# Kernel tuning notes

Measured on AMD Instinct MI355X. Metric: run time of the kernel, lower is better.

Reference implementation:

```python
import jax, jax.numpy as jnp
import numpy as np

N = 100000
E = 1600000
F_IN = 128
HID = 64


def setup_inputs() -> dict:
    key = jax.random.key(0)
    ks = jax.random.split(key, 8)
    x = jax.random.normal(ks[0], (N, F_IN), dtype=jnp.float32)
    edge_index = jax.random.randint(ks[1], (2, E), 0, N, dtype=jnp.int32)
    # GCNConv params: weight [in, out] (glorot-ish scale), bias [out]
    W1 = jax.random.normal(ks[2], (F_IN, HID), dtype=jnp.float32) / np.sqrt(F_IN)
    b1 = jnp.zeros((HID,), dtype=jnp.float32)
    W2 = jax.random.normal(ks[3], (HID, HID), dtype=jnp.float32) / np.sqrt(HID)
    b2 = jnp.zeros((HID,), dtype=jnp.float32)
    Wc = jax.random.normal(ks[4], (HID, 1), dtype=jnp.float32) / np.sqrt(HID)
    bc = jnp.zeros((1,), dtype=jnp.float32)
    return {"x": x, "edge_index": edge_index, "W1": W1, "b1": b1,
            "W2": W2, "b2": b2, "Wc": Wc, "bc": bc}


def _gcn_conv(x, src, dst, W, b):
    # PyG GCNConv: h = x @ W, then symmetric-normalized aggregation over
    # edges with self-loops: out[d] = sum_e deg^-1/2[s] deg^-1/2[d] h[s] + b
    n = x.shape[0]
    h = x @ W                                            # [N, out]
    deg = jax.ops.segment_sum(jnp.ones_like(dst, dtype=h.dtype), dst,
                              num_segments=n)            # in-degree incl. self-loops
    dinv = jnp.where(deg > 0, jax.lax.rsqrt(deg), 0.0)   # [N]
    norm = dinv[src] * dinv[dst]                         # [E+N]
    msg = h[src] * norm[:, None]                         # gather + scale
    out = jax.ops.segment_sum(msg, dst, num_segments=n)  # scatter-add
    return out + b


def reference(x, edge_index, W1, b1, W2, b2, Wc, bc):
    n = x.shape[0]
    loop = jnp.arange(n, dtype=edge_index.dtype)
    src = jnp.concatenate([edge_index[0], loop])  # add self-loops
    dst = jnp.concatenate([edge_index[1], loop])
    h = jax.nn.relu(_gcn_conv(x, src, dst, W1, b1))  # dropout in eval mode = identity
    h = jax.nn.relu(_gcn_conv(h, src, dst, W2, b2))
    return (h @ Wc + bc).squeeze(-1)  # [N]
```

## Files before the change

kernel.cpp:

```cpp
#include <hip/hip_runtime.h>


#define FIN 128
#define HIDDEN 64
#define NBUCK 196
#define CAP 9216
#define EPB 8192

typedef __attribute__((ext_vector_type(8))) short bf16x8;
typedef __attribute__((ext_vector_type(4))) float f32x4;

__device__ __forceinline__ unsigned f2bf_pair(float a, float b) {
    unsigned ua = __float_as_uint(a);
    unsigned ub = __float_as_uint(b);
    ua = (ua + 0x7FFFu + ((ua >> 16) & 1u)) >> 16;
    ub = (ub + 0x7FFFu + ((ub >> 16) & 1u)) & 0xFFFF0000u;
    return ua | ub;
}
__device__ __forceinline__ unsigned short f2bf1(float a) {
    unsigned u = __float_as_uint(a);
    return (unsigned short)((u + 0x7FFFu + ((u >> 16) & 1u)) >> 16);
}
#define BF_LO(u) __uint_as_float((u) << 16)
#define BF_HI(u) __uint_as_float((u) & 0xFFFF0000u)

__global__ __launch_bounds__(256) void k_scatter_direct(const int* __restrict__ src,
                                                        const int* __restrict__ dst,
                                                        int* __restrict__ bcursor,
                                                        int* __restrict__ pairs, int e) {
    __shared__ int h[NBUCK], base_s[NBUCK], cur[NBUCK];
    int dloc[EPB / 256];
    int tid = threadIdx.x;
    if (tid < NBUCK) { h[tid] = 0; cur[tid] = 0; }
    __syncthreads();
    int start = blockIdx.x * EPB;
#pragma unroll
    for (int i = 0; i < EPB / 256; i++) {
        int idx = start + tid + i * 256;
        int d = (idx < e) ? dst[idx] : -1;
        dloc[i] = d;
        if (d >= 0) atomicAdd(&h[d >> 9], 1);
    }
    __syncthreads();
    if (tid < NBUCK && h[tid] > 0) base_s[tid] = atomicAdd(&bcursor[tid], h[tid]);
    __syncthreads();
#pragma unroll
    for (int i = 0; i < EPB / 256; i++) {
        int idx = start + tid + i * 256;
        int d = dloc[i];
        if (d >= 0) {
            int b = d >> 9;
            int pos = base_s[b] + atomicAdd(&cur[b], 1);
            if (pos < CAP) pairs[b * CAP + pos] = (src[idx] << 9) | (d & 511);
        }
    }
}

__global__ __launch_bounds__(256) void k_csr_bucket(const int* __restrict__ pairs,
                                                    const int* __restrict__ bcursor,
                                                    int2* __restrict__ rowinfo,
                                                    float* __restrict__ dinv,
                                                    int* __restrict__ csr_src, int n) {
    __shared__ int cnt[512];
    __shared__ int off[512];
    __shared__ int ws2[256];
    int tid = threadIdx.x;
    int b = blockIdx.x;
    int node0 = b << 9;
    cnt[tid] = 0; cnt[tid + 256] = 0;
    __syncthreads();
    int s0 = b * CAP;
    int s1 = s0 + min(bcursor[b], CAP);
    for (int i = s0 + tid; i < s1; i += 256) atomicAdd(&cnt[pairs[i] & 511], 1);
    __syncthreads();
    int c0 = cnt[2 * tid], c1 = cnt[2 * tid + 1];
    int tsum = c0 + c1;
    ws2[tid] = tsum;
    __syncthreads();
    for (int o = 1; o < 256; o <<= 1) {
        int x = 0;
        if (tid >= o) x = ws2[tid - o];
        __syncthreads();
        if (tid >= o) ws2[tid] += x;
        __syncthreads();
    }
    int excl = ws2[tid] - tsum;
    off[2 * tid] = excl;
    off[2 * tid + 1] = excl + c0;
    int n0 = node0 + 2 * tid, n1 = node0 + 2 * tid + 1;
    if (n0 < n) { rowinfo[n0] = make_int2(s0 + excl, c0);      dinv[n0] = rsqrtf((float)c0 + 1.0f); }
    if (n1 < n) { rowinfo[n1] = make_int2(s0 + excl + c0, c1); dinv[n1] = rsqrtf((float)c1 + 1.0f); }
    cnt[2 * tid] = 0; cnt[2 * tid + 1] = 0;
    __syncthreads();
    for (int i = s0 + tid; i < s1; i += 256) {
        int p = pairs[i];
        int l = p & 511;
        int pos = s0 + off[l] + atomicAdd(&cnt[l], 1);
        csr_src[pos] = p >> 9;
    }
}


__global__ __launch_bounds__(256) void k_mfma1(const float4* __restrict__ x4,
                                               const float* __restrict__ w1,
                                               const float* __restrict__ dinv,
                                               uint2* __restrict__ hsb, int n) {
    __shared__ unsigned short sW[64 * 136];
    int tid = threadIdx.x;
#pragma unroll
    for (int i = 0; i < 32; i++) {
        int idx = tid + i * 256;
        int k = idx >> 6, ch = idx & 63;
        sW[ch * 136 + k] = f2bf1(w1[idx]);
    }
    __syncthreads();
    int lane = tid & 63, wave = tid >> 6;
    int quad = lane >> 4, nl = lane & 15;
    int node = blockIdx.x * 64 + wave * 16 + nl;
    int ic = min(node, n - 1);
    const float4* px = x4 + (size_t)ic * 32 + quad * 2;
    bf16x8 bfr[4];
#pragma unroll
    for (int kc = 0; kc < 4; kc++) {
        float4 p = px[kc * 8];
        float4 q = px[kc * 8 + 1];
        union { unsigned u[4]; bf16x8 v; } t;
        t.u[0] = f2bf_pair(p.x, p.y); t.u[1] = f2bf_pair(p.z, p.w);
        t.u[2] = f2bf_pair(q.x, q.y); t.u[3] = f2bf_pair(q.z, q.w);
        bfr[kc] = t.v;
    }
    const bf16x8* sW8 = (const bf16x8*)sW;
    f32x4 a0 = {0.f, 0.f, 0.f, 0.f}, a1 = a0, a2 = a0, a3 = a0;
#pragma unroll
    for (int kc = 0; kc < 4; kc++) {
        int ko = kc * 4 + quad;
        bf16x8 w0 = sW8[(nl +  0) * 17 + ko];
        bf16x8 w1f = sW8[(nl + 16) * 17 + ko];
        bf16x8 w2f = sW8[(nl + 32) * 17 + ko];
        bf16x8 w3f = sW8[(nl + 48) * 17 + ko];
        a0 = __builtin_amdgcn_mfma_f32_16x16x32_bf16(w0,  bfr[kc], a0, 0, 0, 0);
        a1 = __builtin_amdgcn_mfma_f32_16x16x32_bf16(w1f, bfr[kc], a1, 0, 0, 0);
        a2 = __builtin_amdgcn_mfma_f32_16x16x32_bf16(w2f, bfr[kc], a2, 0, 0, 0);
        a3 = __builtin_amdgcn_mfma_f32_16x16x32_bf16(w3f, bfr[kc], a3, 0, 0, 0);
    }
    if (node < n) {
        float s = dinv[node];
        uint2* o = hsb + (size_t)node * 16 + quad;
        o[0]  = make_uint2(f2bf_pair(a0.x * s, a0.y * s), f2bf_pair(a0.z * s, a0.w * s));
        o[4]  = make_uint2(f2bf_pair(a1.x * s, a1.y * s), f2bf_pair(a1.z * s, a1.w * s));
        o[8]  = make_uint2(f2bf_pair(a2.x * s, a2.y * s), f2bf_pair(a2.z * s, a2.w * s));
        o[12] = make_uint2(f2bf_pair(a3.x * s, a3.y * s), f2bf_pair(a3.z * s, a3.w * s));
    }
}

__global__ __launch_bounds__(256) void k_agg1_gemm2(const int2* __restrict__ rowinfo,
                                                    const int* __restrict__ csr_src,
                                                    const uint4* __restrict__ hsb4,
                                                    const float* __restrict__ dinv,
                                                    const float4* __restrict__ b1_4,
                                                    const float* __restrict__ w2,
                                                    uint2* __restrict__ hsb2, int n) {
    __shared__ unsigned short sW[64 * 72];
    __shared__ float sV[16 * 68];
    int tid = threadIdx.x;
#pragma unroll
    for (int i = 0; i < 16; i++) {
        int idx = tid + i * 256;
        int k = idx >> 6, ch = idx & 63;
        sW[ch * 72 + k] = f2bf1(w2[idx]);
    }
    int lane = tid & 63;
    int node0 = blockIdx.x * 16;
    int nloc = tid >> 4;
    int node = node0 + nloc;
    int el = (lane >> 3) & 1, cq = lane & 7;
    if (node < n) {
        int2 rpd = rowinfo[node];
        int start = rpd.x, deg = rpd.y;
        int end = start + deg;
        float4 accA = make_float4(0.f, 0.f, 0.f, 0.f), accB = accA;
        int nr = (deg + 3) >> 2;
#pragma unroll 2
        for (int r = 0; r < nr; r++) {
            int base = start + (r << 2);
            int e0 = base + el;
            int e1 = base + 2 + el;
            int s0 = csr_src[min(e0, end - 1)];
            int s1 = csr_src[min(e1, end - 1)];
            float m0 = (e0 < end) ? 1.f : 0.f;
            float m1 = (e1 < end) ? 1.f : 0.f;
            uint4 g0 = hsb4[(size_t)s0 * 8 + cq];
            uint4 g1 = hsb4[(size_t)s1 * 8 + cq];
            accA.x += m0 * BF_LO(g0.x) + m1 * BF_LO(g1.x);
            accA.y += m0 * BF_HI(g0.x) + m1 * BF_HI(g1.x);
            accA.z += m0 * BF_LO(g0.y) + m1 * BF_LO(g1.y);
            accA.w += m0 * BF_HI(g0.y) + m1 * BF_HI(g1.y);
            accB.x += m0 * BF_LO(g0.z) + m1 * BF_LO(g1.z);
            accB.y += m0 * BF_HI(g0.z) + m1 * BF_HI(g1.z);
            accB.z += m0 * BF_LO(g0.w) + m1 * BF_LO(g1.w);
            accB.w += m0 * BF_HI(g0.w) + m1 * BF_HI(g1.w);
        }
        accA.x += __shfl_xor(accA.x, 8); accA.y += __shfl_xor(accA.y, 8);
        accA.z += __shfl_xor(accA.z, 8); accA.w += __shfl_xor(accA.w, 8);
        accB.x += __shfl_xor(accB.x, 8); accB.y += __shfl_xor(accB.y, 8);
        accB.z += __shfl_xor(accB.z, 8); accB.w += __shfl_xor(accB.w, 8);
        if (el == 0) {
            uint4 g = hsb4[(size_t)node * 8 + cq];
            float s = dinv[node];
            float4 bA = b1_4[cq * 2], bB = b1_4[cq * 2 + 1];
            float4 vA, vB;
            vA.x = fmaxf(s * (accA.x + BF_LO(g.x)) + bA.x, 0.f);
            vA.y = fmaxf(s * (accA.y + BF_HI(g.x)) + bA.y, 0.f);
            vA.z = fmaxf(s * (accA.z + BF_LO(g.y)) + bA.z, 0.f);
            vA.w = fmaxf(s * (accA.w + BF_HI(g.y)) + bA.w, 0.f);
            vB.x = fmaxf(s * (accB.x + BF_LO(g.z)) + bB.x, 0.f);
            vB.y = fmaxf(s * (accB.y + BF_HI(g.z)) + bB.y, 0.f);
            vB.z = fmaxf(s * (accB.z + BF_LO(g.w)) + bB.z, 0.f);
            vB.w = fmaxf(s * (accB.w + BF_HI(g.w)) + bB.w, 0.f);
            float* vb = sV + nloc * 68 + cq * 8;
            *(float4*)vb = vA;
            *(float4*)(vb + 4) = vB;
        }
    }
    __syncthreads();
    int wave = tid >> 6;
    int quad = lane >> 4, nl = lane & 15;
    const bf16x8* sW8 = (const bf16x8*)sW;
    f32x4 acc = {0.f, 0.f, 0.f, 0.f};
#pragma unroll
    for (int kc = 0; kc < 2; kc++) {
        const float* vb = sV + nl * 68 + kc * 32 + quad * 8;
        float4 p = *(const float4*)vb;
        float4 q = *(const float4*)(vb + 4);
        union { unsigned u[4]; bf16x8 v; } t;
        t.u[0] = f2bf_pair(p.x, p.y); t.u[1] = f2bf_pair(p.z, p.w);
        t.u[2] = f2bf_pair(q.x, q.y); t.u[3] = f2bf_pair(q.z, q.w);
        bf16x8 a = sW8[(wave * 16 + nl) * 9 + kc * 4 + quad];
        acc = __builtin_amdgcn_mfma_f32_16x16x32_bf16(a, t.v, acc, 0, 0, 0);
    }
    int onode = node0 + nl;
    if (onode < n) {
        float s = dinv[onode];
        hsb2[(size_t)onode * 16 + wave * 4 + quad] =
            make_uint2(f2bf_pair(acc.x * s, acc.y * s), f2bf_pair(acc.z * s, acc.w * s));
    }
}

__global__ __launch_bounds__(256) void k_agg2_head(const int2* __restrict__ rowinfo,
                                                   const int* __restrict__ csr_src,
                                                   const uint4* __restrict__ hsb4,
                                                   const float* __restrict__ dinv,
                                                   const float4* __restrict__ b2_4,
                                                   const float4* __restrict__ wc_4,
                                                   const float* __restrict__ bc,
                                                   float* __restrict__ out, int n) {
    int lane = threadIdx.x & 63;
    int node = (blockIdx.x * 256 + threadIdx.x) >> 4;
    if (node >= n) return;
    int el = (lane >> 3) & 1, cq = lane & 7;
    int2 rpd = rowinfo[node];
    int start = rpd.x, deg = rpd.y;
    int end = start + deg;
    float4 accA = make_float4(0.f, 0.f, 0.f, 0.f), accB = accA;
    int nr = (deg + 3) >> 2;
#pragma unroll 2
    for (int r = 0; r < nr; r++) {
        int base = start + (r << 2);
        int e0 = base + el;
        int e1 = base + 2 + el;
        int s0 = csr_src[min(e0, end - 1)];
        int s1 = csr_src[min(e1, end - 1)];
        float m0 = (e0 < end) ? 1.f : 0.f;
        float m1 = (e1 < end) ? 1.f : 0.f;
        uint4 g0 = hsb4[(size_t)s0 * 8 + cq];
        uint4 g1 = hsb4[(size_t)s1 * 8 + cq];
        accA.x += m0 * BF_LO(g0.x) + m1 * BF_LO(g1.x);
        accA.y += m0 * BF_HI(g0.x) + m1 * BF_HI(g1.x);
        accA.z += m0 * BF_LO(g0.y) + m1 * BF_LO(g1.y);
        accA.w += m0 * BF_HI(g0.y) + m1 * BF_HI(g1.y);
        accB.x += m0 * BF_LO(g0.z) + m1 * BF_LO(g1.z);
        accB.y += m0 * BF_HI(g0.z) + m1 * BF_HI(g1.z);
        accB.z += m0 * BF_LO(g0.w) + m1 * BF_LO(g1.w);
        accB.w += m0 * BF_HI(g0.w) + m1 * BF_HI(g1.w);
    }
    accA.x += __shfl_xor(accA.x, 8); accA.y += __shfl_xor(accA.y, 8);
    accA.z += __shfl_xor(accA.z, 8); accA.w += __shfl_xor(accA.w, 8);
    accB.x += __shfl_xor(accB.x, 8); accB.y += __shfl_xor(accB.y, 8);
    accB.z += __shfl_xor(accB.z, 8); accB.w += __shfl_xor(accB.w, 8);
    uint4 g = hsb4[(size_t)node * 8 + cq];
    float s = dinv[node];
    float4 bA = b2_4[cq * 2], bB = b2_4[cq * 2 + 1];
    float4 wA = wc_4[cq * 2], wB = wc_4[cq * 2 + 1];
    float t = fmaxf(s * (accA.x + BF_LO(g.x)) + bA.x, 0.f) * wA.x
            + fmaxf(s * (accA.y + BF_HI(g.x)) + bA.y, 0.f) * wA.y
            + fmaxf(s * (accA.z + BF_LO(g.y)) + bA.z, 0.f) * wA.z
            + fmaxf(s * (accA.w + BF_HI(g.y)) + bA.w, 0.f) * wA.w
            + fmaxf(s * (accB.x + BF_LO(g.z)) + bB.x, 0.f) * wB.x
            + fmaxf(s * (accB.y + BF_HI(g.z)) + bB.y, 0.f) * wB.y
            + fmaxf(s * (accB.z + BF_LO(g.w)) + bB.z, 0.f) * wB.z
            + fmaxf(s * (accB.w + BF_HI(g.w)) + bB.w, 0.f) * wB.w;
    t += __shfl_xor(t, 1);
    t += __shfl_xor(t, 2);
    t += __shfl_xor(t, 4);
    if ((lane & 15) == 0) out[node] = t + bc[0];
}

extern "C" void kernel_launch(void* const* d_in, const int* in_sizes, int n_in,
                              void* d_out, int out_size, void* d_ws, size_t ws_size,
                              hipStream_t stream) {
    const float* x  = (const float*)d_in[0];
    const int*   ei = (const int*)d_in[1];
    const float* W1 = (const float*)d_in[2];
    const float* b1 = (const float*)d_in[3];
    const float* W2 = (const float*)d_in[4];
    const float* b2 = (const float*)d_in[5];
    const float* Wc = (const float*)d_in[6];
    const float* bc = (const float*)d_in[7];
    int n = in_sizes[0] / FIN;
    int e = in_sizes[1] / 2;
    const int* srcv = ei;
    const int* dstv = ei + e;

    char* ws = (char*)d_ws;
    float* dinv    = (float*)(ws + 0);
    int2*  rowinfo = (int2*)(ws + (512u << 10));
    int*   csr_src = (int*)(ws + 1536u * 1024);
    int*   bcursor = (int*)(ws + 8800u * 1024);
    uint2* hsb1    = (uint2*)(ws + (9u << 20));
    uint2* hsb2    = (uint2*)(ws + (22u << 20));
    int*   pairs   = (int*)hsb2;

    int nb_sc   = (e + EPB - 1) / EPB;
    int nb_rows = (n + 63) / 64;
    int nb_agg  = (n + 15) / 16;

    hipMemsetAsync(bcursor, 0, NBUCK * sizeof(int), stream);
    k_scatter_direct<<<nb_sc, 256, 0, stream>>>(srcv, dstv, bcursor, pairs, e);
    k_csr_bucket<<<NBUCK, 256, 0, stream>>>(pairs, bcursor, rowinfo, dinv, csr_src, n);

    k_mfma1<<<nb_rows, 256, 0, stream>>>((const float4*)x, W1, dinv, hsb1, n);
    k_agg1_gemm2<<<nb_agg, 256, 0, stream>>>(rowinfo, csr_src, (const uint4*)hsb1,
                                             dinv, (const float4*)b1, W2, hsb2, n);
    k_agg2_head<<<nb_agg, 256, 0, stream>>>(rowinfo, csr_src, (const uint4*)hsb2,
                                            dinv, (const float4*)b2, (const float4*)Wc,
                                            bc, (float*)d_out, n);
}
```

Baseline: 215.9 us.

## Fuse edge scatter with first GEMM, move dinv scaling into aggregation

The edge bucketing scatter and the first x@W1 MFMA GEMM now run in one launch, with block ranges split by role. This is possible because the GEMM no longer pre-scales rows by dinv; instead the layer-1 aggregation gathers dinv[src] per edge and applies s^2 to the self term. Buckets shrink to 256 nodes (more buckets, smaller capacity), and both aggregation loops are unrolled to four neighbours per lane-pair per iteration. The goal is to overlap the GEMM with the scatter, remove a launch, and raise memory-level parallelism in the gathers, at the cost of an extra dinv gather per edge in layer 1.

Measured after the change: 211.0 us. 2.3% less time.

```diff
diff --git a/kernel.cpp b/kernel.cpp
--- a/kernel.cpp
+++ b/kernel.cpp
@@ -3,9 +3,9 @@
 
 #define FIN 128
 #define HIDDEN 64
-#define NBUCK 196
-#define CAP 9216
-#define EPB 8192
+#define NBUCK 391
+#define CAP 4608
+#define EPB 4096
 
 typedef __attribute__((ext_vector_type(8))) short bf16x8;
 typedef __attribute__((ext_vector_type(4))) float f32x4;
@@ -24,89 +24,48 @@
 #define BF_LO(u) __uint_as_float((u) << 16)
 #define BF_HI(u) __uint_as_float((u) & 0xFFFF0000u)
 
-__global__ __launch_bounds__(256) void k_scatter_direct(const int* __restrict__ src,
-                                                        const int* __restrict__ dst,
-                                                        int* __restrict__ bcursor,
-                                                        int* __restrict__ pairs, int e) {
-    __shared__ int h[NBUCK], base_s[NBUCK], cur[NBUCK];
-    int dloc[EPB / 256];
+__global__ __launch_bounds__(256) void k_scatter_mfma1(const int* __restrict__ src,
+                                                       const int* __restrict__ dst,
+                                                       int* __restrict__ bcursor,
+                                                       int* __restrict__ pairs, int e,
+                                                       const float4* __restrict__ x4,
+                                                       const float* __restrict__ w1,
+                                                       uint2* __restrict__ hsb,
+                                                       int n, int nsc) {
+    __shared__ int sbuf[4352];
     int tid = threadIdx.x;
-    if (tid < NBUCK) { h[tid] = 0; cur[tid] = 0; }
-    __syncthreads();
-    int start = blockIdx.x * EPB;
-#pragma unroll
-    for (int i = 0; i < EPB / 256; i++) {
-        int idx = start + tid + i * 256;
-        int d = (idx < e) ? dst[idx] : -1;
-        dloc[i] = d;
-        if (d >= 0) atomicAdd(&h[d >> 9], 1);
-    }
-    __syncthreads();
-    if (tid < NBUCK && h[tid] > 0) base_s[tid] = atomicAdd(&bcursor[tid], h[tid]);
-    __syncthreads();
-#pragma unroll
-    for (int i = 0; i < EPB / 256; i++) {
-        int idx = start + tid + i * 256;
-        int d = dloc[i];
-        if (d >= 0) {
-            int b = d >> 9;
-            int pos = base_s[b] + atomicAdd(&cur[b], 1);
-            if (pos < CAP) pairs[b * CAP + pos] = (src[idx] << 9) | (d & 511);
+    if ((int)blockIdx.x < nsc) {
+        int* h      = sbuf;
+        int* base_s = sbuf + NBUCK;
+        int* cur    = sbuf + 2 * NBUCK;
+        int dloc[EPB / 256];
+        for (int i = tid; i < NBUCK; i += 256) { h[i] = 0; cur[i] = 0; }
+        __syncthreads();
+        int start = blockIdx.x * EPB;
+#pragma unroll
+        for (int i = 0; i < EPB / 256; i++) {
+            int idx = start + tid + i * 256;
+            int d = (idx < e) ? dst[idx] : -1;
+            dloc[i] = d;
+            if (d >= 0) atomicAdd(&h[d >> 8], 1);
         }
-    }
-}
-
-__global__ __launch_bounds__(256) void k_csr_bucket(const int* __restrict__ pairs,
-                                                    const int* __restrict__ bcursor,
-                                                    int2* __restrict__ rowinfo,
-                                                    float* __restrict__ dinv,
-                                                    int* __restrict__ csr_src, int n) {
-    __shared__ int cnt[512];
-    __shared__ int off[512];
-    __shared__ int ws2[256];
-    int tid = threadIdx.x;
-    int b = blockIdx.x;
-    int node0 = b << 9;
-    cnt[tid] = 0; cnt[tid + 256] = 0;
-    __syncthreads();
-    int s0 = b * CAP;
-    int s1 = s0 + min(bcursor[b], CAP);
-    for (int i = s0 + tid; i < s1; i += 256) atomicAdd(&cnt[pairs[i] & 511], 1);
-    __syncthreads();
-    int c0 = cnt[2 * tid], c1 = cnt[2 * tid + 1];
-    int tsum = c0 + c1;
-    ws2[tid] = tsum;
-    __syncthreads();
-    for (int o = 1; o < 256; o <<= 1) {
-        int x = 0;
-        if (tid >= o) x = ws2[tid - o];
-        __syncthreads();
-        if (tid >= o) ws2[tid] += x;
-        __syncthreads();
-    }
-    int excl = ws2[tid] - tsum;
-    off[2 * tid] = excl;
-    off[2 * tid + 1] = excl + c0;
-    int n0 = node0 + 2 * tid, n1 = node0 + 2 * tid + 1;
-    if (n0 < n) { rowinfo[n0] = make_int2(s0 + excl, c0);      dinv[n0] = rsqrtf((float)c0 + 1.0f); }
-    if (n1 < n) { rowinfo[n1] = make_int2(s0 + excl + c0, c1); dinv[n1] = rsqrtf((float)c1 + 1.0f); }
-    cnt[2 * tid] = 0; cnt[2 * tid + 1] = 0;
-    __syncthreads();
-    for (int i = s0 + tid; i < s1; i += 256) {
-        int p = pairs[i];
-        int l = p & 511;
-        int pos = s0 + off[l] + atomicAdd(&cnt[l], 1);
-        csr_src[pos] = p >> 9;
-    }
-}
-
-
-__global__ __launch_bounds__(256) void k_mfma1(const float4* __restrict__ x4,
-                                               const float* __restrict__ w1,
-                                               const float* __restrict__ dinv,
-                                               uint2* __restrict__ hsb, int n) {
-    __shared__ unsigned short sW[64 * 136];
-    int tid = threadIdx.x;
+        __syncthreads();
+        for (int i = tid; i < NBUCK; i += 256)
+            if (h[i] > 0) base_s[i] = atomicAdd(&bcursor[i], h[i]);
+        __syncthreads();
+#pragma unroll
+        for (int i = 0; i < EPB / 256; i++) {
+            int idx = start + tid + i * 256;
+            int d = dloc[i];
+            if (d >= 0) {
+                int b = d >> 8;
+                int pos = base_s[b] + atomicAdd(&cur[b], 1);
+                if (pos < CAP) pairs[b * CAP + pos] = (src[idx] << 8) | (d & 255);
+            }
+        }
+        return;
+    }
+    unsigned short* sW = (unsigned short*)sbuf;
 #pragma unroll
     for (int i = 0; i < 32; i++) {
         int idx = tid + i * 256;
@@ -116,7 +75,7 @@
     __syncthreads();
     int lane = tid & 63, wave = tid >> 6;
     int quad = lane >> 4, nl = lane & 15;
-    int node = blockIdx.x * 64 + wave * 16 + nl;
+    int node = (blockIdx.x - nsc) * 64 + wave * 16 + nl;
     int ic = min(node, n - 1);
     const float4* px = x4 + (size_t)ic * 32 + quad * 2;
     bf16x8 bfr[4];
@@ -144,12 +103,55 @@
         a3 = __builtin_amdgcn_mfma_f32_16x16x32_bf16(w3f, bfr[kc], a3, 0, 0, 0);
     }
     if (node < n) {
-        float s = dinv[node];
         uint2* o = hsb + (size_t)node * 16 + quad;
-        o[0]  = make_uint2(f2bf_pair(a0.x * s, a0.y * s), f2bf_pair(a0.z * s, a0.w * s));
-        o[4]  = make_uint2(f2bf_pair(a1.x * s, a1.y * s), f2bf_pair(a1.z * s, a1.w * s));
-        o[8]  = make_uint2(f2bf_pair(a2.x * s, a2.y * s), f2bf_pair(a2.z * s, a2.w * s));
-        o[12] = make_uint2(f2bf_pair(a3.x * s, a3.y * s), f2bf_pair(a3.z * s, a3.w * s));
+        o[0]  = make_uint2(f2bf_pair(a0.x, a0.y), f2bf_pair(a0.z, a0.w));
+        o[4]  = make_uint2(f2bf_pair(a1.x, a1.y), f2bf_pair(a1.z, a1.w));
+        o[8]  = make_uint2(f2bf_pair(a2.x, a2.y), f2bf_pair(a2.z, a2.w));
+        o[12] = make_uint2(f2bf_pair(a3.x, a3.y), f2bf_pair(a3.z, a3.w));
+    }
+}
+
+__global__ __launch_bounds__(256) void k_csr_bucket(const int* __restrict__ pairs,
+                                                    const int* __restrict__ bcursor,
+                                                    int2* __restrict__ rowinfo,
+                                                    float* __restrict__ dinv,
+                                                    int* __restrict__ csr_src, int n) {
+    __shared__ int cnt[256];
+    __shared__ int off[256];
+    __shared__ int ws[256];
+    int tid = threadIdx.x;
+    int b = blockIdx.x;
+    int node0 = b << 8;
+    cnt[tid] = 0;
+    __syncthreads();
+    int s0 = b * CAP;
+    int s1 = s0 + min(bcursor[b], CAP);
+    for (int i = s0 + tid; i < s1; i += 256) atomicAdd(&cnt[pairs[i] & 255], 1);
+    __syncthreads();
+    int c = cnt[tid];
+    ws[tid] = c;
+    __syncthreads();
+    for (int o = 1; o < 256; o <<= 1) {
+        int x = 0;
+        if (tid >= o) x = ws[tid - o];
+        __syncthreads();
+        ws[tid] += x;
+        __syncthreads();
+    }
+    int excl = ws[tid] - c;
+    off[tid] = excl;
+    int node = node0 + tid;
+    if (node < n) {
+        rowinfo[node] = make_int2(s0 + excl, c);
+        dinv[node] = rsqrtf((float)c + 1.0f);
+    }
+    cnt[tid] = 0;
+    __syncthreads();
+    for (int i = s0 + tid; i < s1; i += 256) {
+        int p = pairs[i];
+        int l = p & 255;
+        int pos = s0 + off[l] + atomicAdd(&cnt[l], 1);
+        csr_src[pos] = p >> 8;
     }
 }
 
@@ -179,26 +181,30 @@
         int start = rpd.x, deg = rpd.y;
         int end = start + deg;
         float4 accA = make_float4(0.f, 0.f, 0.f, 0.f), accB = accA;
-        int nr = (deg + 3) >> 2;
-#pragma unroll 2
+        int nr = (deg + 7) >> 3;
         for (int r = 0; r < nr; r++) {
-            int base = start + (r << 2);
-            int e0 = base + el;
-            int e1 = base + 2 + el;
+            int base = start + (r << 3) + el;
+            int e0 = base, e1 = base + 2, e2 = base + 4, e3 = base + 6;
             int s0 = csr_src[min(e0, end - 1)];
             int s1 = csr_src[min(e1, end - 1)];
-            float m0 = (e0 < end) ? 1.f : 0.f;
-            float m1 = (e1 < end) ? 1.f : 0.f;
+            int s2 = csr_src[min(e2, end - 1)];
+            int s3 = csr_src[min(e3, end - 1)];
+            float m0 = (e0 < end) ? dinv[s0] : 0.f;
+            float m1 = (e1 < end) ? dinv[s1] : 0.f;
+            float m2 = (e2 < end) ? dinv[s2] : 0.f;
+            float m3 = (e3 < end) ? dinv[s3] : 0.f;
             uint4 g0 = hsb4[(size_t)s0 * 8 + cq];
             uint4 g1 = hsb4[(size_t)s1 * 8 + cq];
-            accA.x += m0 * BF_LO(g0.x) + m1 * BF_LO(g1.x);
-            accA.y += m0 * BF_HI(g0.x) + m1 * BF_HI(g1.x);
-            accA.z += m0 * BF_LO(g0.y) + m1 * BF_LO(g1.y);
-            accA.w += m0 * BF_HI(g0.y) + m1 * BF_HI(g1.y);
-            accB.x += m0 * BF_LO(g0.z) + m1 * BF_LO(g1.z);
-            accB.y += m0 * BF_HI(g0.z) + m1 * BF_HI(g1.z);
-            accB.z += m0 * BF_LO(g0.w) + m1 * BF_LO(g1.w);
-            accB.w += m0 * BF_HI(g0.w) + m1 * BF_HI(g1.w);
+            uint4 g2 = hsb4[(size_t)s2 * 8 + cq];
+            uint4 g3 = hsb4[(size_t)s3 * 8 + cq];
+            accA.x += m0 * BF_LO(g0.x) + m1 * BF_LO(g1.x) + m2 * BF_LO(g2.x) + m3 * BF_LO(g3.x);
+            accA.y += m0 * BF_HI(g0.x) + m1 * BF_HI(g1.x) + m2 * BF_HI(g2.x) + m3 * BF_HI(g3.x);
+            accA.z += m0 * BF_LO(g0.y) + m1 * BF_LO(g1.y) + m2 * BF_LO(g2.y) + m3 * BF_LO(g3.y);
+            accA.w += m0 * BF_HI(g0.y) + m1 * BF_HI(g1.y) + m2 * BF_HI(g2.y) + m3 * BF_HI(g3.y);
+            accB.x += m0 * BF_LO(g0.z) + m1 * BF_LO(g1.z) + m2 * BF_LO(g2.z) + m3 * BF_LO(g3.z);
+            accB.y += m0 * BF_HI(g0.z) + m1 * BF_HI(g1.z) + m2 * BF_HI(g2.z) + m3 * BF_HI(g3.z);
+            accB.z += m0 * BF_LO(g0.w) + m1 * BF_LO(g1.w) + m2 * BF_LO(g2.w) + m3 * BF_LO(g3.w);
+            accB.w += m0 * BF_HI(g0.w) + m1 * BF_HI(g1.w) + m2 * BF_HI(g2.w) + m3 * BF_HI(g3.w);
         }
         accA.x += __shfl_xor(accA.x, 8); accA.y += __shfl_xor(accA.y, 8);
         accA.z += __shfl_xor(accA.z, 8); accA.w += __shfl_xor(accA.w, 8);
@@ -207,16 +213,17 @@
         if (el == 0) {
             uint4 g = hsb4[(size_t)node * 8 + cq];
             float s = dinv[node];
+            float sq = s * s;
             float4 bA = b1_4[cq * 2], bB = b1_4[cq * 2 + 1];
             float4 vA, vB;
-            vA.x = fmaxf(s * (accA.x + BF_LO(g.x)) + bA.x, 0.f);
-            vA.y = fmaxf(s * (accA.y + BF_HI(g.x)) + bA.y, 0.f);
-            vA.z = fmaxf(s * (accA.z + BF_LO(g.y)) + bA.z, 0.f);
-            vA.w = fmaxf(s * (accA.w + BF_HI(g.y)) + bA.w, 0.f);
-            vB.x = fmaxf(s * (accB.x + BF_LO(g.z)) + bB.x, 0.f);
-            vB.y = fmaxf(s * (accB.y + BF_HI(g.z)) + bB.y, 0.f);
-            vB.z = fmaxf(s * (accB.z + BF_LO(g.w)) + bB.z, 0.f);
-            vB.w = fmaxf(s * (accB.w + BF_HI(g.w)) + bB.w, 0.f);
+            vA.x = fmaxf(s * accA.x + sq * BF_LO(g.x) + bA.x, 0.f);
+            vA.y = fmaxf(s * accA.y + sq * BF_HI(g.x) + bA.y, 0.f);
+            vA.z = fmaxf(s * accA.z + sq * BF_LO(g.y) + bA.z, 0.f);
+            vA.w = fmaxf(s * accA.w + sq * BF_HI(g.y) + bA.w, 0.f);
+            vB.x = fmaxf(s * accB.x + sq * BF_LO(g.z) + bB.x, 0.f);
+            vB.y = fmaxf(s * accB.y + sq * BF_HI(g.z) + bB.y, 0.f);
+            vB.z = fmaxf(s * accB.z + sq * BF_LO(g.w) + bB.z, 0.f);
+            vB.w = fmaxf(s * accB.w + sq * BF_HI(g.w) + bB.w, 0.f);
             float* vb = sV + nloc * 68 + cq * 8;
             *(float4*)vb = vA;
             *(float4*)(vb + 4) = vB;
@@ -262,26 +269,30 @@
     int start = rpd.x, deg = rpd.y;
     int end = start + deg;
     float4 accA = make_float4(0.f, 0.f, 0.f, 0.f), accB = accA;
-    int nr = (deg + 3) >> 2;
-#pragma unroll 2
+    int nr = (deg + 7) >> 3;
     for (int r = 0; r < nr; r++) {
-        int base = start + (r << 2);
-        int e0 = base + el;
-        int e1 = base + 2 + el;
+        int base = start + (r << 3) + el;
+        int e0 = base, e1 = base + 2, e2 = base + 4, e3 = base + 6;
         int s0 = csr_src[min(e0, end - 1)];
         int s1 = csr_src[min(e1, end - 1)];
+        int s2 = csr_src[min(e2, end - 1)];
+        int s3 = csr_src[min(e3, end - 1)];
         float m0 = (e0 < end) ? 1.f : 0.f;
         float m1 = (e1 < end) ? 1.f : 0.f;
+        float m2 = (e2 < end) ? 1.f : 0.f;
+        float m3 = (e3 < end) ? 1.f : 0.f;
         uint4 g0 = hsb4[(size_t)s0 * 8 + cq];
         uint4 g1 = hsb4[(size_t)s1 * 8 + cq];
-        accA.x += m0 * BF_LO(g0.x) + m1 * BF_LO(g1.x);
-        accA.y += m0 * BF_HI(g0.x) + m1 * BF_HI(g1.x);
-        accA.z += m0 * BF_LO(g0.y) + m1 * BF_LO(g1.y);
-        accA.w += m0 * BF_HI(g0.y) + m1 * BF_HI(g1.y);
-        accB.x += m0 * BF_LO(g0.z) + m1 * BF_LO(g1.z);
-        accB.y += m0 * BF_HI(g0.z) + m1 * BF_HI(g1.z);
-        accB.z += m0 * BF_LO(g0.w) + m1 * BF_LO(g1.w);
-        accB.w += m0 * BF_HI(g0.w) + m1 * BF_HI(g1.w);
+        uint4 g2 = hsb4[(size_t)s2 * 8 + cq];
+        uint4 g3 = hsb4[(size_t)s3 * 8 + cq];
+        accA.x += m0 * BF_LO(g0.x) + m1 * BF_LO(g1.x) + m2 * BF_LO(g2.x) + m3 * BF_LO(g3.x);
+        accA.y += m0 * BF_HI(g0.x) + m1 * BF_HI(g1.x) + m2 * BF_HI(g2.x) + m3 * BF_HI(g3.x);
+        accA.z += m0 * BF_LO(g0.y) + m1 * BF_LO(g1.y) + m2 * BF_LO(g2.y) + m3 * BF_LO(g3.y);
+        accA.w += m0 * BF_HI(g0.y) + m1 * BF_HI(g1.y) + m2 * BF_HI(g2.y) + m3 * BF_HI(g3.y);
+        accB.x += m0 * BF_LO(g0.z) + m1 * BF_LO(g1.z) + m2 * BF_LO(g2.z) + m3 * BF_LO(g3.z);
+        accB.y += m0 * BF_HI(g0.z) + m1 * BF_HI(g1.z) + m2 * BF_HI(g2.z) + m3 * BF_HI(g3.z);
+        accB.z += m0 * BF_LO(g0.w) + m1 * BF_LO(g1.w) + m2 * BF_LO(g2.w) + m3 * BF_LO(g3.w);
+        accB.w += m0 * BF_HI(g0.w) + m1 * BF_HI(g1.w) + m2 * BF_HI(g2.w) + m3 * BF_HI(g3.w);
     }
     accA.x += __shfl_xor(accA.x, 8); accA.y += __shfl_xor(accA.y, 8);
     accA.z += __shfl_xor(accA.z, 8); accA.w += __shfl_xor(accA.w, 8);
@@ -335,10 +346,10 @@
     int nb_agg  = (n + 15) / 16;
 
     hipMemsetAsync(bcursor, 0, NBUCK * sizeof(int), stream);
-    k_scatter_direct<<<nb_sc, 256, 0, stream>>>(srcv, dstv, bcursor, pairs, e);
+    k_scatter_mfma1<<<nb_sc + nb_rows, 256, 0, stream>>>(srcv, dstv, bcursor, pairs, e,
+                                                         (const float4*)x, W1, hsb1,
+                                                         n, nb_sc);
     k_csr_bucket<<<NBUCK, 256, 0, stream>>>(pairs, bcursor, rowinfo, dinv, csr_src, n);
-
-    k_mfma1<<<nb_rows, 256, 0, stream>>>((const float4*)x, W1, dinv, hsb1, n);
     k_agg1_gemm2<<<nb_agg, 256, 0, stream>>>(rowinfo, csr_src, (const uint4*)hsb1,
                                              dinv, (const float4*)b1, W2, hsb2, n);
     k_agg2_head<<<nb_agg, 256, 0, stream>>>(rowinfo, csr_src, (const uint4*)hsb2,
```
